# Kernel tuning notes

Hardware: AMD Instinct MI355X
Metric: run time of the kernel (lower is better)

## Reference

```python
import jax, jax.numpy as jnp
import numpy as np

BDY = 8  # relative positions clipped to [-8, 8] -> 17 bins


def setup_inputs() -> dict:
    key = jax.random.key(0)
    ks = jax.random.split(key, 7)
    B, L, H, A, P = 2, 256, 256, 32, 64
    return {
        "inputs_embeds": jax.random.normal(ks[0], (B, L, H), dtype=jnp.float32),
        "in_w": jax.random.normal(ks[1], (A, H), dtype=jnp.float32) * (H ** -0.5),
        "in_b": jax.random.normal(ks[2], (A,), dtype=jnp.float32) * 0.02,
        "out_w": jax.random.normal(ks[3], (P, A * A), dtype=jnp.float32) * ((A * A) ** -0.5),
        "out_b": jax.random.normal(ks[4], (P,), dtype=jnp.float32) * 0.02,
        "pos_w": jax.random.normal(ks[5], (P, 17), dtype=jnp.float32) * 0.1,
        "pos_b": jax.random.normal(ks[6], (P,), dtype=jnp.float32) * 0.02,
    }


def reference(inputs_embeds, in_w, in_b, out_w, out_b, pos_w, pos_b):
    B, L, _ = inputs_embeds.shape
    A = in_w.shape[0]
    # in_proj: [B, L, A]
    h = jnp.einsum("blh,ah->bla", inputs_embeds, in_w) + in_b
    # outer product over sequence positions and channels: [B, Li, Lj, A, A]
    tri = jnp.einsum("bia,bjc->bijac", h, h).reshape(B, L, L, A * A)
    # out_proj: [B, Li, Lj, P]
    out = jnp.einsum("bijk,pk->bijp", tri, out_w) + out_b
    # relative-position embedding: one-hot(clip(i-j)) @ pos_w^T == gather rows
    pos = jnp.arange(L)
    d = jnp.clip(pos[:, None] - pos[None, :], -BDY, BDY) + BDY  # [L, L] in [0, 16]
    pos_emb = pos_w.T[d] + pos_b  # [L, L, P]
    return out + pos_emb[None]
```

## Files before the change

kernel.cpp:

```cpp
#include <hip/hip_runtime.h>

#define B_ 2
#define L_ 256
#define H_ 256
#define A_ 32
#define P_ 64
#define PSTR 76
#define TSTR 516
#define XSTR 260

typedef __bf16 bf16x8 __attribute__((ext_vector_type(8)));
typedef float  f32x4  __attribute__((ext_vector_type(4)));

__global__ __launch_bounds__(256) void k1_proj(
    const float* __restrict__ x,
    const float* __restrict__ in_w,
    const float* __restrict__ in_b,
    const float* __restrict__ out_w,
    __bf16* __restrict__ gb,
    __bf16* __restrict__ hb)
{
    __shared__ float xs[8][XSTR];
    __shared__ float ws[32][XSTR];
    __shared__ float hl[8][A_];

    const int t = threadIdx.x;
    const int rowg = blockIdx.x >> 3;
    const int pe   = blockIdx.x & 7;
    const int r0 = rowg * 8;

    #pragma unroll
    for (int u = t; u < 512; u += 256) {
        const int row = u >> 6, c4 = u & 63;
        *(float4*)&xs[row][c4 * 4] = ((const float4*)(x + (size_t)(r0 + row) * H_))[c4];
    }
    #pragma unroll
    for (int u = t; u < 2048; u += 256) {
        const int a = u >> 6, c4 = u & 63;
        *(float4*)&ws[a][c4 * 4] = ((const float4*)(in_w + (size_t)a * H_))[c4];
    }
    __syncthreads();

    {
        const int row = t >> 5, a = t & 31;
        float s = 0.f;
        #pragma unroll
        for (int c4 = 0; c4 < 64; ++c4) {
            const float4 xv = *(const float4*)&xs[row][c4 * 4];
            const float4 wv = *(const float4*)&ws[a][c4 * 4];
            s += xv.x * wv.x + xv.y * wv.y + xv.z * wv.z + xv.w * wv.w;
        }
        const float hv = s + in_b[a];
        hl[row][a] = hv;
        if (pe == 0) hb[(size_t)(r0 + row) * A_ + a] = (__bf16)hv;
    }
    __syncthreads();

    {
        const int p = pe * 8 + (t >> 5);
        const int a = t & 31;
        const float4* wrow = (const float4*)(out_w + (size_t)p * (A_ * A_) + a * A_);
        float4 w[8];
        #pragma unroll
        for (int m = 0; m < 8; ++m) w[m] = wrow[m];
        float sac[8];
        #pragma unroll
        for (int jj = 0; jj < 8; ++jj) {
            const float4* hh = (const float4*)hl[jj];
            float s = 0.f;
            #pragma unroll
            for (int m = 0; m < 8; ++m) {
                const float4 h4 = hh[m];
                s += w[m].x * h4.x + w[m].y * h4.y + w[m].z * h4.z + w[m].w * h4.w;
            }
            sac[jj] = s;
        }
        #pragma unroll
        for (int jj = 0; jj < 8; ++jj)
            gb[((size_t)(r0 + jj) * P_ + p) * A_ + a] = (__bf16)sac[jj];
    }
}

__global__ __launch_bounds__(256) void k2_mfma(
    const __bf16* __restrict__ gb,
    const __bf16* __restrict__ hb,
    const float* __restrict__ out_b,
    const float* __restrict__ pos_w,
    const float* __restrict__ pos_b,
    float* __restrict__ out)
{
    __shared__ float posT[17 * PSTR];
    __shared__ float tile[16][TSTR];
    const int t = threadIdx.x;

    for (int e = t; e < 17 * P_; e += 256) {
        const int d = e >> 6, p = e & 63;
        posT[d * PSTR + p] = pos_w[p * 17 + d] + pos_b[p] + out_b[p];
    }
    __syncthreads();

    const int lane = t & 63;
    const int w = t >> 6;
    const int j0 = blockIdx.x * 8;
    const int i0 = blockIdx.y * 16;
    const int b = blockIdx.z;

    const int l15 = lane & 15;
    const int hi = lane >> 4;
    const int i = i0 + l15;
    const int p_r0 = hi * 4;

    const bf16x8 hfrag = *(const bf16x8*)(hb + ((size_t)(b * L_ + i)) * A_ + hi * 8);
    const f32x4 zero = {0.f, 0.f, 0.f, 0.f};

    #pragma unroll
    for (int tj = 0; tj < 2; ++tj) {
        const int jl = w * 2 + tj;
        const int j = j0 + jl;
        const __bf16* gr = gb + ((size_t)(b * L_ + j)) * (P_ * A_);

        bf16x8 gfrag[4];
        #pragma unroll
        for (int pg = 0; pg < 4; ++pg)
            gfrag[pg] = *(const bf16x8*)(gr + (pg * 16 + l15) * A_ + hi * 8);

        f32x4 acc[4];
        #pragma unroll
        for (int pg = 0; pg < 4; ++pg)
            acc[pg] = __builtin_amdgcn_mfma_f32_16x16x32_bf16(gfrag[pg], hfrag, zero, 0, 0, 0);

        int d = i - j;
        d = d < -8 ? -8 : (d > 8 ? 8 : d);
        d += 8;

        #pragma unroll
        for (int pg = 0; pg < 4; ++pg) {
            const f32x4 pe = *(const f32x4*)(posT + d * PSTR + pg * 16 + p_r0);
            *(f32x4*)&tile[l15][jl * 64 + pg * 16 + p_r0] = acc[pg] + pe;
        }
    }
    __syncthreads();

    const int ir = t >> 4;
    const int c  = t & 15;
    float* orow = out + (((size_t)(b * L_ + i0 + ir)) * L_ + j0) * P_;
    #pragma unroll
    for (int m = 0; m < 8; ++m) {
        const int f4 = m * 16 + c;
        const f32x4 v = *(const f32x4*)&tile[ir][f4 * 4];
        __builtin_nontemporal_store(v, (f32x4*)(orow + f4 * 4));
    }
}

extern "C" void kernel_launch(void* const* d_in, const int* in_sizes, int n_in,
                              void* d_out, int out_size, void* d_ws, size_t ws_size,
                              hipStream_t stream) {
    const float* x     = (const float*)d_in[0];
    const float* in_w  = (const float*)d_in[1];
    const float* in_b  = (const float*)d_in[2];
    const float* out_w = (const float*)d_in[3];
    const float* out_b = (const float*)d_in[4];
    const float* pos_w = (const float*)d_in[5];
    const float* pos_b = (const float*)d_in[6];
    float* out = (float*)d_out;

    __bf16* gb = (__bf16*)d_ws;
    __bf16* hb = gb + (size_t)B_ * L_ * P_ * A_;

    k1_proj<<<dim3(512), 256, 0, stream>>>(x, in_w, in_b, out_w, gb, hb);
    k2_mfma<<<dim3(L_ / 8, L_ / 16, B_), 256, 0, stream>>>(gb, hb, out_b, pos_w, pos_b, out);
}
```

Before: 21.49 us.

## Split in_proj reduction across threads and process two j-tiles per k2 block

In k1, the in_w staging through shared memory is dropped. Each thread now loads a quarter of one in_w row into registers, computes partial dot products for four x rows, and the partials are reduced through shared memory. This cuts LDS traffic and the footprint of the large ws buffer. In k2, each block now handles two 8-column j tiles, halving the grid and amortizing the posT table setup and the hfrag load across more work. The hfrag load is also moved ahead of the barrier. The cost is an extra barrier per sub-tile and fewer blocks available for parallelism.

```diff
diff --git a/kernel.cpp b/kernel.cpp
--- a/kernel.cpp
+++ b/kernel.cpp
@@ -21,8 +21,8 @@
     __bf16* __restrict__ hb)
 {
     __shared__ float xs[8][XSTR];
-    __shared__ float ws[32][XSTR];
-    __shared__ float hl[8][A_];
+    __shared__ float hp[4][8][33];
+    __shared__ float hl[8][36];
 
     const int t = threadIdx.x;
     const int rowg = blockIdx.x >> 3;
@@ -34,23 +34,41 @@
         const int row = u >> 6, c4 = u & 63;
         *(float4*)&xs[row][c4 * 4] = ((const float4*)(x + (size_t)(r0 + row) * H_))[c4];
     }
-    #pragma unroll
-    for (int u = t; u < 2048; u += 256) {
-        const int a = u >> 6, c4 = u & 63;
-        *(float4*)&ws[a][c4 * 4] = ((const float4*)(in_w + (size_t)a * H_))[c4];
+    __syncthreads();
+
+    {
+        const int a  = t & 31;
+        const int r4 = (t >> 5) & 1;
+        const int q  = t >> 6;
+        float4 wq[16];
+        const float4* wr = (const float4*)(in_w + (size_t)a * H_ + q * 64);
+        #pragma unroll
+        for (int m = 0; m < 16; ++m) wq[m] = wr[m];
+
+        float s0 = 0.f, s1 = 0.f, s2 = 0.f, s3 = 0.f;
+        #pragma unroll
+        for (int m = 0; m < 16; ++m) {
+            const float4 w = wq[m];
+            const float4 x0 = *(const float4*)&xs[r4 * 4 + 0][q * 64 + m * 4];
+            const float4 x1 = *(const float4*)&xs[r4 * 4 + 1][q * 64 + m * 4];
+            const float4 x2 = *(const float4*)&xs[r4 * 4 + 2][q * 64 + m * 4];
+            const float4 x3 = *(const float4*)&xs[r4 * 4 + 3][q * 64 + m * 4];
+            s0 += w.x * x0.x + w.y * x0.y + w.z * x0.z + w.w * x0.w;
+            s1 += w.x * x1.x + w.y * x1.y + w.z * x1.z + w.w * x1.w;
+            s2 += w.x * x2.x + w.y * x2.y + w.z * x2.z + w.w * x2.w;
+            s3 += w.x * x3.x + w.y * x3.y + w.z * x3.z + w.w * x3.w;
+        }
+        hp[q][r4 * 4 + 0][a] = s0;
+        hp[q][r4 * 4 + 1][a] = s1;
+        hp[q][r4 * 4 + 2][a] = s2;
+        hp[q][r4 * 4 + 3][a] = s3;
     }
     __syncthreads();
 
     {
         const int row = t >> 5, a = t & 31;
-        float s = 0.f;
-        #pragma unroll
-        for (int c4 = 0; c4 < 64; ++c4) {
-            const float4 xv = *(const float4*)&xs[row][c4 * 4];
-            const float4 wv = *(const float4*)&ws[a][c4 * 4];
-            s += xv.x * wv.x + xv.y * wv.y + xv.z * wv.z + xv.w * wv.w;
-        }
-        const float hv = s + in_b[a];
+        const float hv = ((hp[0][row][a] + hp[1][row][a]) +
+                          (hp[2][row][a] + hp[3][row][a])) + in_b[a];
         hl[row][a] = hv;
         if (pe == 0) hb[(size_t)(r0 + row) * A_ + a] = (__bf16)hv;
     }
@@ -66,11 +84,10 @@
         float sac[8];
         #pragma unroll
         for (int jj = 0; jj < 8; ++jj) {
-            const float4* hh = (const float4*)hl[jj];
             float s = 0.f;
             #pragma unroll
             for (int m = 0; m < 8; ++m) {
-                const float4 h4 = hh[m];
+                const float4 h4 = *(const float4*)&hl[jj][m * 4];
                 s += w[m].x * h4.x + w[m].y * h4.y + w[m].z * h4.z + w[m].w * h4.w;
             }
             sac[jj] = s;
@@ -97,11 +114,9 @@
         const int d = e >> 6, p = e & 63;
         posT[d * PSTR + p] = pos_w[p * 17 + d] + pos_b[p] + out_b[p];
     }
-    __syncthreads();
 
     const int lane = t & 63;
     const int w = t >> 6;
-    const int j0 = blockIdx.x * 8;
     const int i0 = blockIdx.y * 16;
     const int b = blockIdx.z;
 
@@ -112,43 +127,52 @@
 
     const bf16x8 hfrag = *(const bf16x8*)(hb + ((size_t)(b * L_ + i)) * A_ + hi * 8);
     const f32x4 zero = {0.f, 0.f, 0.f, 0.f};
+    __syncthreads();
 
     #pragma unroll
-    for (int tj = 0; tj < 2; ++tj) {
-        const int jl = w * 2 + tj;
-        const int j = j0 + jl;
-        const __bf16* gr = gb + ((size_t)(b * L_ + j)) * (P_ * A_);
-
-        bf16x8 gfrag[4];
-        #pragma unroll
-        for (int pg = 0; pg < 4; ++pg)
-            gfrag[pg] = *(const bf16x8*)(gr + (pg * 16 + l15) * A_ + hi * 8);
-
-        f32x4 acc[4];
-        #pragma unroll
-        for (int pg = 0; pg < 4; ++pg)
-            acc[pg] = __builtin_amdgcn_mfma_f32_16x16x32_bf16(gfrag[pg], hfrag, zero, 0, 0, 0);
-
-        int d = i - j;
-        d = d < -8 ? -8 : (d > 8 ? 8 : d);
-        d += 8;
+    for (int sub = 0; sub < 2; ++sub) {
+        const int j0 = (blockIdx.x * 2 + sub) * 8;
 
         #pragma unroll
-        for (int pg = 0; pg < 4; ++pg) {
-            const f32x4 pe = *(const f32x4*)(posT + d * PSTR + pg * 16 + p_r0);
-            *(f32x4*)&tile[l15][jl * 64 + pg * 16 + p_r0] = acc[pg] + pe;
+        for (int tj = 0; tj < 2; ++tj) {
+            const int jl = w * 2 + tj;
+            const int j = j0 + jl;
+            const __bf16* gr = gb + ((size_t)(b * L_ + j)) * (P_ * A_);
+
+            bf16x8 gfrag[4];
+            #pragma unroll
+            for (int pg = 0; pg < 4; ++pg)
+                gfrag[pg] = *(const bf16x8*)(gr + (pg * 16 + l15) * A_ + hi * 8);
+
+            f32x4 acc[4];
+            #pragma unroll
+            for (int pg = 0; pg < 4; ++pg)
+                acc[pg] = __builtin_amdgcn_mfma_f32_16x16x32_bf16(gfrag[pg], hfrag, zero, 0, 0, 0);
+
+            int d = i - j;
+            d = d < -8 ? -8 : (d > 8 ? 8 : d);
+            d += 8;
+
+            #pragma unroll
+            for (int pg = 0; pg < 4; ++pg) {
+                const f32x4 pe = *(const f32x4*)(posT + d * PSTR + pg * 16 + p_r0);
+                *(f32x4*)&tile[l15][jl * 64 + pg * 16 + p_r0] = acc[pg] + pe;
+            }
         }
-    }
-    __syncthreads();
+        __syncthreads();
 
-    const int ir = t >> 4;
-    const int c  = t & 15;
-    float* orow = out + (((size_t)(b * L_ + i0 + ir)) * L_ + j0) * P_;
-    #pragma unroll
-    for (int m = 0; m < 8; ++m) {
-        const int f4 = m * 16 + c;
-        const f32x4 v = *(const f32x4*)&tile[ir][f4 * 4];
-        __builtin_nontemporal_store(v, (f32x4*)(orow + f4 * 4));
+        {
+            const int ir = t >> 4;
+            const int c  = t & 15;
+            float* orow = out + (((size_t)(b * L_ + i0 + ir)) * L_ + j0) * P_;
+            #pragma unroll
+            for (int m = 0; m < 8; ++m) {
+                const int f4 = m * 16 + c;
+                const f32x4 v = *(const f32x4*)&tile[ir][f4 * 4];
+                __builtin_nontemporal_store(v, (f32x4*)(orow + f4 * 4));
+            }
+        }
+        __syncthreads();
     }
 }
 
@@ -168,5 +192,5 @@
     __bf16* hb = gb + (size_t)B_ * L_ * P_ * A_;
 
     k1_proj<<<dim3(512), 256, 0, stream>>>(x, in_w, in_b, out_w, gb, hb);
-    k2_mfma<<<dim3(L_ / 8, L_ / 16, B_), 256, 0, stream>>>(gb, hb, out_b, pos_w, pos_b, out);
+    k2_mfma<<<dim3(16, 16, B_), 256, 0, stream>>>(gb, hb, out_b, pos_w, pos_b, out);
 }
```

After: 22.81 us. 6.2% more time.
